# Kernel optimization log

Hardware: AMD Instinct MI355X
Metric: run time of the kernel (lower is better)

## Reference

```python
import jax, jax.numpy as jnp
import numpy as np

N, E = 50000, 800000          # nodes, edges
IN, H, C = 256, 4, 64          # in_channels, heads, per-head out channels
HID, OUT = 64, 40              # lin1 hidden, num classes
NEG_SLOPE = 0.2                # PyG GATConv default


def setup_inputs() -> dict:
    key = jax.random.key(0)
    ks = jax.random.split(key, 10)
    s = 0.05
    return {
        "x": jax.random.normal(ks[0], (N, IN), jnp.float32),
        "edge_index": jax.random.randint(ks[1], (2, E), 0, N, dtype=jnp.int64),
        "W": jax.random.normal(ks[2], (IN, H * C), jnp.float32) * s,     # GATConv lin (no bias)
        "att_src": jax.random.normal(ks[3], (H, C), jnp.float32) * s,
        "att_dst": jax.random.normal(ks[4], (H, C), jnp.float32) * s,
        "bias_conv": jnp.zeros((H * C,), jnp.float32),
        "W1": jax.random.normal(ks[5], (H * C, HID), jnp.float32) * s,
        "b1": jnp.zeros((HID,), jnp.float32),
        "W2": jax.random.normal(ks[6], (HID, OUT), jnp.float32) * s,
        "b2": jnp.zeros((OUT,), jnp.float32),
    }


def reference(x, edge_index, W, att_src, att_dst, bias_conv, W1, b1, W2, b2):
    n = x.shape[0]
    # PyG GATConv default: add self-loops (also guarantees no empty segments)
    loop = jnp.arange(n, dtype=edge_index.dtype)
    src = jnp.concatenate([edge_index[0], loop])  # [E+N]
    dst = jnp.concatenate([edge_index[1], loop])

    h = (x @ W).reshape(n, H, C)                         # [N,H,C]
    a_src = jnp.einsum('nhc,hc->nh', h, att_src)         # [N,H]
    a_dst = jnp.einsum('nhc,hc->nh', h, att_dst)

    # per-edge attention logits + segment softmax over incoming edges of dst
    e = jax.nn.leaky_relu(a_src[src] + a_dst[dst], NEG_SLOPE)   # [E+N,H]
    m = jax.ops.segment_max(e, dst, num_segments=n)             # [N,H]
    ex = jnp.exp(e - m[dst])
    denom = jax.ops.segment_sum(ex, dst, num_segments=n)
    alpha = ex / denom[dst]                                     # [E+N,H]

    # weighted scatter-aggregate of source features
    msg = alpha[:, :, None] * h[src]                            # [E+N,H,C]
    out = jax.ops.segment_sum(msg, dst, num_segments=n)         # [N,H,C]
    out = out.reshape(n, H * C) + bias_conv

    out = jax.nn.relu(out)              # .relu() after conv1 (dropout off in eval)
    out = jax.nn.relu(out @ W1 + b1)    # lin1 + relu
    return out @ W2 + b2                # lin2
```

## Files before the change

### kernel.cpp

```cpp
#include <hip/hip_runtime.h>
#include <math.h>

#define HEADS 4
#define CH 64
#define HC 256
#define SLOPE 0.2f
#define SLOT 64

typedef __attribute__((ext_vector_type(8))) short bf16x8;
typedef __attribute__((ext_vector_type(8))) unsigned short u16x8;
typedef __attribute__((ext_vector_type(4))) float f32x4;

__device__ __forceinline__ float4 ld4(const float* p){ return *(const float4*)p; }
__device__ __forceinline__ void st4(float* p, float4 v){ *(float4*)p = v; }
__device__ __forceinline__ float lrelu(float x){ return x > 0.f ? x : SLOPE * x; }
__device__ __forceinline__ unsigned short f2bf(float f){
  union { float f; unsigned int u; } v; v.f = f;
  unsigned int r = v.u + 0x7fffu + ((v.u >> 16) & 1u);
  return (unsigned short)(r >> 16);
}
__device__ __forceinline__ float bflo(unsigned int u){
  union { unsigned int u; float f; } v; v.u = u << 16; return v.f;
}
__device__ __forceinline__ float bfhi(unsigned int u){
  union { unsigned int u; float f; } v; v.u = u & 0xffff0000u; return v.f;
}
__device__ __forceinline__ void split2(float v, unsigned short& h, unsigned short& l){
  unsigned int u = __float_as_uint(v);
  h = (unsigned short)(u >> 16);
  float hf = __uint_as_float(u & 0xffff0000u);
  l = (unsigned short)(__float_as_uint(v - hf) >> 16);
}
__device__ __forceinline__ void dma16(const unsigned short* g, unsigned short* l){
  __builtin_amdgcn_global_load_lds(
      (const __attribute__((address_space(1))) unsigned int*)g,
      (__attribute__((address_space(3))) unsigned int*)l, 16, 0, 0);
}

__global__ __launch_bounds__(256) void k_pre(
    const float* __restrict__ W, const float* __restrict__ W1, const float* __restrict__ W2,
    unsigned short* __restrict__ Bhi, unsigned short* __restrict__ Blo,
    unsigned short* __restrict__ W1h, unsigned short* __restrict__ W1l,
    unsigned short* __restrict__ W2h, unsigned short* __restrict__ W2l,
    int* __restrict__ cnt, int Nn) {
  int b = blockIdx.x, t = threadIdx.x;
  if (b < 256) {
    int nn = b;
    unsigned short h, l;
    split2(W[(size_t)t*256 + nn], h, l);
    Bhi[(size_t)nn*256 + t] = h; Blo[(size_t)nn*256 + t] = l;
  } else if (b < 320) {
    int nn = b - 256;
    unsigned short h, l;
    split2(W1[(size_t)t*64 + nn], h, l);
    W1h[(size_t)nn*256 + t] = h; W1l[(size_t)nn*256 + t] = l;
  } else if (b < 368) {
    if (t < 64) {
      int nn = b - 320;
      float v = (nn < 40) ? W2[(size_t)t*40 + nn] : 0.f;
      unsigned short h, l;
      split2(v, h, l);
      W2h[(size_t)nn*64 + t] = h; W2l[(size_t)nn*64 + t] = l;
    }
  } else {
    int i = (b - 368)*256 + t;
    if (i < Nn) cnt[i] = 0;
  }
}

__global__ __launch_bounds__(256, 4) void k_gemmfill(const float* __restrict__ x,
    const unsigned short* __restrict__ Bhi_t, const unsigned short* __restrict__ Blo_t,
    unsigned short* __restrict__ hbf,
    const float* __restrict__ att_src, const float* __restrict__ att_dst,
    float* __restrict__ a_srcO, float* __restrict__ a_dstO, int M, int nFill,
    const int* __restrict__ ei, int* __restrict__ cnt, unsigned short* __restrict__ csrf,
    int E, int EN) {
  __shared__ __align__(16) unsigned short L[4*4096];
  int t = threadIdx.x;
  int b = blockIdx.x;
  if (b < nFill) {
    int base = b*2048 + t;
    int s0=0,d0=0,s1=0,d1=0,s2=0,d2=0,s3=0,d3=0;
    int s4=0,d4=0,s5=0,d5=0,s6=0,d6=0,s7=0,d7=0;
    int e0=base, e1=base+256, e2=base+512, e3=base+768;
    int e4=base+1024, e5=base+1280, e6=base+1536, e7=base+1792;
    bool q0=e0<EN,q1=e1<EN,q2=e2<EN,q3=e3<EN,q4=e4<EN,q5=e5<EN,q6=e6<EN,q7=e7<EN;
    if (q0) { if (e0<E) { s0=ei[e0]; d0=ei[E+e0]; } else { s0=e0-E; d0=s0; } }
    if (q1) { if (e1<E) { s1=ei[e1]; d1=ei[E+e1]; } else { s1=e1-E; d1=s1; } }
    if (q2) { if (e2<E) { s2=ei[e2]; d2=ei[E+e2]; } else { s2=e2-E; d2=s2; } }
    if (q3) { if (e3<E) { s3=ei[e3]; d3=ei[E+e3]; } else { s3=e3-E; d3=s3; } }
    if (q4) { if (e4<E) { s4=ei[e4]; d4=ei[E+e4]; } else { s4=e4-E; d4=s4; } }
    if (q5) { if (e5<E) { s5=ei[e5]; d5=ei[E+e5]; } else { s5=e5-E; d5=s5; } }
    if (q6) { if (e6<E) { s6=ei[e6]; d6=ei[E+e6]; } else { s6=e6-E; d6=s6; } }
    if (q7) { if (e7<E) { s7=ei[e7]; d7=ei[E+e7]; } else { s7=e7-E; d7=s7; } }
    if (q0) { int p = atomicAdd(&cnt[d0], 1); csrf[(d0<<6) + p] = (unsigned short)s0; }
    if (q1) { int p = atomicAdd(&cnt[d1], 1); csrf[(d1<<6) + p] = (unsigned short)s1; }
    if (q2) { int p = atomicAdd(&cnt[d2], 1); csrf[(d2<<6) + p] = (unsigned short)s2; }
    if (q3) { int p = atomicAdd(&cnt[d3], 1); csrf[(d3<<6) + p] = (unsigned short)s3; }
    if (q4) { int p = atomicAdd(&cnt[d4], 1); csrf[(d4<<6) + p] = (unsigned short)s4; }
    if (q5) { int p = atomicAdd(&cnt[d5], 1); csrf[(d5<<6) + p] = (unsigned short)s5; }
    if (q6) { int p = atomicAdd(&cnt[d6], 1); csrf[(d6<<6) + p] = (unsigned short)s6; }
    if (q7) { int p = atomicAdd(&cnt[d7], 1); csrf[(d7<<6) + p] = (unsigned short)s7; }
    return;
  }
  int gb = b - nFill;
  int lane = t & 63, w = t >> 6;
  int wr = w >> 1, wc = w & 1;
  int ln15 = lane & 15, lq = lane >> 4;
  int row0 = (gb >> 1) * 128, col0 = (gb & 1) * 128;

  f32x4 acc[4][4];
  #pragma unroll
  for (int i=0;i<4;i++)
    #pragma unroll
    for (int j=0;j<4;j++) acc[i][j] = (f32x4){0.f,0.f,0.f,0.f};

  int sA = w*128 + lane;
  int sB = sA + 64;
  int RA = sA>>3, uA = (sA&7)^(RA&7), idxA = (RA<<1)|(uA&1), segA = uA>>1;
  int RB = sB>>3, uB = (sB&7)^(RB&7), idxB = (RB<<1)|(uB&1), segB = uB>>1;
  size_t gB_a = (size_t)(col0+idxA)*256 + segA*8;
  size_t gB_b = (size_t)(col0+idxB)*256 + segB*8;
  int l0 = (w*128)*8, l1 = (w*128+64)*8;

  int ar = t >> 1, akh = t & 1;
  int arow = row0 + ar;
  bool avalid = arow < M;
  const float* xp = &x[(size_t)arow*256 + akh*16];
  int aR = ar >> 1;
  int u0w = ((2*akh+0) << 1) | (ar & 1);
  int u1w = ((2*akh+1) << 1) | (ar & 1);
  int as0 = aR*8 + (u0w ^ (aR & 7));
  int as1 = aR*8 + (u1w ^ (aR & 7));

  for (int c = 0; c < 8; c++) {
    int k0 = c*32;
    dma16(Bhi_t + gB_a + k0, &L[2*4096 + l0]);
    dma16(Bhi_t + gB_b + k0, &L[2*4096 + l1]);
    dma16(Blo_t + gB_a + k0, &L[3*4096 + l0]);
    dma16(Blo_t + gB_b + k0, &L[3*4096 + l1]);
    float4 f0 = make_float4(0,0,0,0), f1 = f0, f2 = f0, f3 = f0;
    if (avalid) {
      const float* xc = xp + k0;
      f0 = ld4(xc); f1 = ld4(xc+4); f2 = ld4(xc+8); f3 = ld4(xc+12);
    }
    u16x8 h0, l0v, h1, l1v;
    unsigned short hh, ll;
    split2(f0.x,hh,ll); h0[0]=hh; l0v[0]=ll;
    split2(f0.y,hh,ll); h0[1]=hh; l0v[1]=ll;
    split2(f0.z,hh,ll); h0[2]=hh; l0v[2]=ll;
    split2(f0.w,hh,ll); h0[3]=hh; l0v[3]=ll;
    split2(f1.x,hh,ll); h0[4]=hh; l0v[4]=ll;
    split2(f1.y,hh,ll); h0[5]=hh; l0v[5]=ll;
    split2(f1.z,hh,ll); h0[6]=hh; l0v[6]=ll;
    split2(f1.w,hh,ll); h0[7]=hh; l0v[7]=ll;
    split2(f2.x,hh,ll); h1[0]=hh; l1v[0]=ll;
    split2(f2.y,hh,ll); h1[1]=hh; l1v[1]=ll;
    split2(f2.z,hh,ll); h1[2]=hh; l1v[2]=ll;
    split2(f2.w,hh,ll); h1[3]=hh; l1v[3]=ll;
    split2(f3.x,hh,ll); h1[4]=hh; l1v[4]=ll;
    split2(f3.y,hh,ll); h1[5]=hh; l1v[5]=ll;
    split2(f3.z,hh,ll); h1[6]=hh; l1v[6]=ll;
    split2(f3.w,hh,ll); h1[7]=hh; l1v[7]=ll;
    *(u16x8*)&L[0*4096 + as0*8] = h0;
    *(u16x8*)&L[1*4096 + as0*8] = l0v;
    *(u16x8*)&L[0*4096 + as1*8] = h1;
    *(u16x8*)&L[1*4096 + as1*8] = l1v;
    __syncthreads();

    bf16x8 bh[4], bl[4];
    #pragma unroll
    for (int j = 0; j < 4; j++) {
      int nn = wc*64 + j*16 + ln15;
      int R = nn >> 1, u = (lq << 1) | (nn & 1);
      int s = R*8 + (u ^ (R & 7));
      bh[j] = *(bf16x8*)&L[2*4096 + s*8];
      bl[j] = *(bf16x8*)&L[3*4096 + s*8];
    }
    #pragma unroll
    for (int i = 0; i < 4; i++) {
      int r = wr*64 + i*16 + ln15;
      int R = r >> 1, u = (lq << 1) | (r & 1);
      int s = R*8 + (u ^ (R & 7));
      bf16x8 ah = *(bf16x8*)&L[0*4096 + s*8];
      bf16x8 al = *(bf16x8*)&L[1*4096 + s*8];
      #pragma unroll
      for (int j = 0; j < 4; j++) {
        acc[i][j] = __builtin_amdgcn_mfma_f32_16x16x32_bf16(ah, bh[j], acc[i][j], 0,0,0);
        acc[i][j] = __builtin_amdgcn_mfma_f32_16x16x32_bf16(al, bh[j], acc[i][j], 0,0,0);
        acc[i][j] = __builtin_amdgcn_mfma_f32_16x16x32_bf16(ah, bl[j], acc[i][j], 0,0,0);
      }
    }
    __syncthreads();
  }
  unsigned short* hb2 = hbf + (size_t)(gb & 1) * M * 128;
  #pragma unroll
  for (int i = 0; i < 4; i++) {
    #pragma unroll
    for (int r = 0; r < 4; r++) {
      int row = row0 + wr*64 + i*16 + lq*4 + r;
      if (row < M) {
        #pragma unroll
        for (int j = 0; j < 4; j++) {
          int col = wc*64 + j*16 + ln15;
          hb2[(size_t)row*128 + col] = f2bf(acc[i][j][r]);
        }
      }
    }
  }
  int head = (gb & 1)*2 + wc;
  float asv[4], adv[4];
  #pragma unroll
  for (int j=0;j<4;j++){
    asv[j] = att_src[head*CH + j*16 + ln15];
    adv[j] = att_dst[head*CH + j*16 + ln15];
  }
  #pragma unroll
  for (int i = 0; i < 4; i++) {
    #pragma unroll
    for (int r = 0; r < 4; r++) {
      float ps = acc[i][0][r]*asv[0] + acc[i][1][r]*asv[1]
               + acc[i][2][r]*asv[2] + acc[i][3][r]*asv[3];
      float pd = acc[i][0][r]*adv[0] + acc[i][1][r]*adv[1]
               + acc[i][2][r]*adv[2] + acc[i][3][r]*adv[3];
      #pragma unroll
      for (int m=8; m>=1; m>>=1) { ps += __shfl_xor(ps, m); pd += __shfl_xor(pd, m); }
      if (ln15 == 0) {
        int row = row0 + wr*64 + i*16 + lq*4 + r;
        if (row < M) { a_srcO[row*4+head] = ps; a_dstO[row*4+head] = pd; }
      }
    }
  }
}

__global__ __launch_bounds__(256) void k_gat(const unsigned short* __restrict__ hbf,
    const float* __restrict__ a_src, const float* __restrict__ a_dst,
    const int* __restrict__ cnt, const unsigned short* __restrict__ csrf,
    const float* __restrict__ bias, unsigned short* __restrict__ outbf,
    int N, int nBlk) {
  int w = threadIdx.x >> 6, lane = threadIdx.x & 63;
  int q = lane >> 4, cl = lane & 15;
  int pass = (blockIdx.x >= nBlk) ? 1 : 0;
  int blk = blockIdx.x - pass*nBlk;
  int n = blk*16 + w*4 + q;
  int c0 = cl * 8;
  int hd = cl >> 3;
  int eb = q * 16;
  const unsigned short* hb = hbf + (size_t)pass * N * 128;
  const unsigned short* row = &csrf[(size_t)n << 6];

  __shared__ float s_p[4][64][2];

  float2 ad = *(const float2*)&a_dst[(size_t)n*4 + pass*2];
  float dsum = 0.f;
  float acc[8];
  #pragma unroll
  for (int k=0;k<8;k++) acc[k]=0.f;

  int deg = cnt[n];
  int dm = max(deg, __shfl_xor(deg, 16));
  dm = max(dm, __shfl_xor(dm, 32));

  for (int cb = 0; cb < dm; cb += 16) {
    int cnt16 = min(16, deg - cb);
    int cm  = min(16, dm - cb);
    int s = 0;
    float p0 = 0.f, p1 = 0.f;
    if (cl < cnt16) {
      s = row[cb + cl];
      float2 as = *(const float2*)&a_src[(size_t)s*4 + pass*2];
      p0 = __expf(lrelu(as.x + ad.x));
      p1 = __expf(lrelu(as.y + ad.y));
    }
    *(float2*)&s_p[w][eb + cl][0] = make_float2(p0, p1);

    bool v0 = 0 < cnt16, v1 = 1 < cnt16, v2 = 2 < cnt16, v3 = 3 < cnt16;
    uint4 u0 = make_uint4(0,0,0,0), u1 = u0, u2 = u0, u3 = u0;
    int ss;
    ss = __shfl(s, eb + 0); if (v0) u0 = *(const uint4*)&hb[(size_t)ss*128 + c0];
    ss = __shfl(s, eb + 1); if (v1) u1 = *(const uint4*)&hb[(size_t)ss*128 + c0];
    ss = __shfl(s, eb + 2); if (v2) u2 = *(const uint4*)&hb[(size_t)ss*128 + c0];
    ss = __shfl(s, eb + 3); if (v3) u3 = *(const uint4*)&hb[(size_t)ss*128 + c0];
    for (int g = 0; g < cm; g += 4) {
      int f0 = g+4, f1 = g+5, f2 = g+6, f3 = g+7;
      bool w0 = f0 < cnt16, w1 = f1 < cnt16, w2 = f2 < cnt16, w3 = f3 < cnt16;
      uint4 t0 = make_uint4(0,0,0,0), t1 = t0, t2 = t0, t3 = t0;
      ss = __shfl(s, eb + (f0 & 15)); if (w0) t0 = *(const uint4*)&hb[(size_t)ss*128 + c0];
      ss = __shfl(s, eb + (f1 & 15)); if (w1) t1 = *(const uint4*)&hb[(size_t)ss*128 + c0];
      ss = __shfl(s, eb + (f2 & 15)); if (w2) t2 = *(const uint4*)&hb[(size_t)ss*128 + c0];
      ss = __shfl(s, eb + (f3 & 15)); if (w3) t3 = *(const uint4*)&hb[(size_t)ss*128 + c0];
      if (v0) {
        float pw = s_p[w][eb + g    ][hd]; dsum += pw;
        acc[0] += pw*bflo(u0.x); acc[1] += pw*bfhi(u0.x);
        acc[2] += pw*bflo(u0.y); acc[3] += pw*bfhi(u0.y);
        acc[4] += pw*bflo(u0.z); acc[5] += pw*bfhi(u0.z);
        acc[6] += pw*bflo(u0.w); acc[7] += pw*bfhi(u0.w);
      }
      if (v1) {
        float pw = s_p[w][eb + g + 1][hd]; dsum += pw;
        acc[0] += pw*bflo(u1.x); acc[1] += pw*bfhi(u1.x);
        acc[2] += pw*bflo(u1.y); acc[3] += pw*bfhi(u1.y);
        acc[4] += pw*bflo(u1.z); acc[5] += pw*bfhi(u1.z);
        acc[6] += pw*bflo(u1.w); acc[7] += pw*bfhi(u1.w);
      }
      if (v2) {
        float pw = s_p[w][eb + g + 2][hd]; dsum += pw;
        acc[0] += pw*bflo(u2.x); acc[1] += pw*bfhi(u2.x);
        acc[2] += pw*bflo(u2.y); acc[3] += pw*bfhi(u2.y);
        acc[4] += pw*bflo(u2.z); acc[5] += pw*bfhi(u2.z);
        acc[6] += pw*bflo(u2.w); acc[7] += pw*bfhi(u2.w);
      }
      if (v3) {
        float pw = s_p[w][eb + g + 3][hd]; dsum += pw;
        acc[0] += pw*bflo(u3.x); acc[1] += pw*bfhi(u3.x);
        acc[2] += pw*bflo(u3.y); acc[3] += pw*bfhi(u3.y);
        acc[4] += pw*bflo(u3.z); acc[5] += pw*bfhi(u3.z);
        acc[6] += pw*bflo(u3.w); acc[7] += pw*bfhi(u3.w);
      }
      u0 = t0; u1 = t1; u2 = t2; u3 = t3;
      v0 = w0; v1 = w1; v2 = w2; v3 = w3;
    }
  }
  float inv = 1.f / dsum;
  float4 b0 = ld4(&bias[pass*128 + c0]);
  float4 b1 = ld4(&bias[pass*128 + c0 + 4]);
  uint4 o;
  o.x = (unsigned)f2bf(fmaxf(acc[0]*inv + b0.x, 0.f))
      | ((unsigned)f2bf(fmaxf(acc[1]*inv + b0.y, 0.f)) << 16);
  o.y = (unsigned)f2bf(fmaxf(acc[2]*inv + b0.z, 0.f))
      | ((unsigned)f2bf(fmaxf(acc[3]*inv + b0.w, 0.f)) << 16);
  o.z = (unsigned)f2bf(fmaxf(acc[4]*inv + b1.x, 0.f))
      | ((unsigned)f2bf(fmaxf(acc[5]*inv + b1.y, 0.f)) << 16);
  o.w = (unsigned)f2bf(fmaxf(acc[6]*inv + b1.z, 0.f))
      | ((unsigned)f2bf(fmaxf(acc[7]*inv + b1.w, 0.f)) << 16);
  *(uint4*)&outbf[(size_t)n*HC + pass*128 + c0] = o;
}

__global__ __launch_bounds__(256) void k_mlp(const unsigned short* __restrict__ Cbf,
    const unsigned short* __restrict__ W1h, const unsigned short* __restrict__ W1l,
    const unsigned short* __restrict__ W2h, const unsigned short* __restrict__ W2l,
    const float* __restrict__ b1, const float* __restrict__ b2,
    float* __restrict__ out, int M) {
  __shared__ __align__(16) unsigned short Hs[64*72];
  int t = threadIdx.x, lane = t & 63, w = t >> 6;
  int ln15 = lane & 15, lq = lane >> 4;
  int row0 = blockIdx.x * 64;
  int arow = row0 + w*16 + ln15;

  bf16x8 a[8];
  bool av = arow < M;
  const unsigned short* ap = &Cbf[(size_t)arow*256 + lq*8];
  #pragma unroll
  for (int kf = 0; kf < 8; kf++) {
    if (av) a[kf] = *(const bf16x8*)(ap + kf*32);
    else    a[kf] = (bf16x8){0,0,0,0,0,0,0,0};
  }

  f32x4 acc1[4];
  #pragma unroll
  for (int j=0;j<4;j++) acc1[j] = (f32x4){0.f,0.f,0.f,0.f};

  #pragma unroll
  for (int kf = 0; kf < 8; kf++) {
    int k = kf*32 + lq*8;
    #pragma unroll
    for (int j = 0; j < 4; j++) {
      int n = j*16 + ln15;
      bf16x8 bh = *(const bf16x8*)&W1h[(size_t)n*256 + k];
      bf16x8 bl = *(const bf16x8*)&W1l[(size_t)n*256 + k];
      acc1[j] = __builtin_amdgcn_mfma_f32_16x16x32_bf16(a[kf], bh, acc1[j], 0,0,0);
      acc1[j] = __builtin_amdgcn_mfma_f32_16x16x32_bf16(a[kf], bl, acc1[j], 0,0,0);
    }
  }
  #pragma unroll
  for (int j = 0; j < 4; j++) {
    int col = j*16 + ln15;
    float bv = b1[col];
    #pragma unroll
    for (int r = 0; r < 4; r++) {
      int rl = w*16 + lq*4 + r;
      Hs[rl*72 + col] = f2bf(fmaxf(acc1[j][r] + bv, 0.f));
    }
  }
  __syncthreads();
  f32x4 acc2[3];
  #pragma unroll
  for (int j=0;j<3;j++) acc2[j] = (f32x4){0.f,0.f,0.f,0.f};
  #pragma unroll
  for (int kf = 0; kf < 2; kf++) {
    int m = w*16 + ln15;
    bf16x8 a2 = *(bf16x8*)&Hs[m*72 + kf*32 + lq*8];
    #pragma unroll
    for (int j = 0; j < 3; j++) {
      int n = j*16 + ln15;
      int k = kf*32 + lq*8;
      bf16x8 wh = *(const bf16x8*)&W2h[(size_t)n*64 + k];
      bf16x8 wl = *(const bf16x8*)&W2l[(size_t)n*64 + k];
      acc2[j] = __builtin_amdgcn_mfma_f32_16x16x32_bf16(a2, wh, acc2[j], 0,0,0);
      acc2[j] = __builtin_amdgcn_mfma_f32_16x16x32_bf16(a2, wl, acc2[j], 0,0,0);
    }
  }
  #pragma unroll
  for (int j = 0; j < 3; j++) {
    int col = j*16 + ln15;
    if (col < 40) {
      float bv = b2[col];
      #pragma unroll
      for (int r = 0; r < 4; r++) {
        int row = row0 + w*16 + lq*4 + r;
        if (row < M) out[(size_t)row*40 + col] = acc2[j][r] + bv;
      }
    }
  }
}

extern "C" void kernel_launch(void* const* d_in, const int* in_sizes, int n_in,
                              void* d_out, int out_size, void* d_ws, size_t ws_size,
                              hipStream_t stream) {
  const int Nn = in_sizes[0] / HC;
  const int E  = in_sizes[1] / 2;
  const int Mpad = (Nn + 127) & ~127;
  const float* x        = (const float*)d_in[0];
  const int*   ei       = (const int*)d_in[1];
  const float* W        = (const float*)d_in[2];
  const float* att_src  = (const float*)d_in[3];
  const float* att_dst  = (const float*)d_in[4];
  const float* biasconv = (const float*)d_in[5];
  const float* W1       = (const float*)d_in[6];
  const float* b1       = (const float*)d_in[7];
  const float* W2       = (const float*)d_in[8];
  const float* b2       = (const float*)d_in[9];
  float* out = (float*)d_out;

  size_t off = 0;
  auto alloc = [&](size_t bytes)->void* {
    void* p = (void*)((char*)d_ws + off);
    off += (bytes + 255) & ~(size_t)255;
    return p;
  };
  unsigned short* hbf  = (unsigned short*)alloc((size_t)Nn*HC*sizeof(unsigned short));
  unsigned short* outc = (unsigned short*)alloc((size_t)Mpad*HC*sizeof(unsigned short));
  unsigned short* Bhi = (unsigned short*)alloc((size_t)256*256*sizeof(unsigned short));
  unsigned short* Blo = (unsigned short*)alloc((size_t)256*256*sizeof(unsigned short));
  unsigned short* W1h = (unsigned short*)alloc((size_t)64*256*sizeof(unsigned short));
  unsigned short* W1l = (unsigned short*)alloc((size_t)64*256*sizeof(unsigned short));
  unsigned short* W2h = (unsigned short*)alloc((size_t)48*64*sizeof(unsigned short));
  unsigned short* W2l = (unsigned short*)alloc((size_t)48*64*sizeof(unsigned short));
  float* a_src_v  = (float*)alloc((size_t)Nn*4*sizeof(float));
  float* a_dst_v  = (float*)alloc((size_t)Nn*4*sizeof(float));
  int*   cnt      = (int*)alloc((size_t)Nn*sizeof(int));
  unsigned short* csrf = (unsigned short*)alloc((size_t)Nn*SLOT*sizeof(unsigned short));
  (void)ws_size; (void)n_in; (void)out_size;

  dim3 blk(256);
  int nGemm = 2 * (Mpad/128);
  int EN = E + Nn;
  int nFill = (EN + 2047)/2048;
  int nZero = (Nn + 255)/256;
  int nBlkGat = Nn/16;

  k_pre<<<dim3(368 + nZero), blk, 0, stream>>>(W, W1, W2,
      Bhi, Blo, W1h, W1l, W2h, W2l, cnt, Nn);
  k_gemmfill<<<dim3(nFill + nGemm), blk, 0, stream>>>(x, Bhi, Blo, hbf,
      att_src, att_dst, a_src_v, a_dst_v, Nn, nFill, ei, cnt, csrf, E, EN);
  k_gat<<<dim3(2*nBlkGat), blk, 0, stream>>>(hbf, a_src_v, a_dst_v,
                                             cnt, csrf, biasconv, outc, Nn, nBlkGat);
  k_mlp<<<dim3((Mpad + 63)/64), blk, 0, stream>>>(outc, W1h, W1l, W2h, W2l, b1, b2, out, Nn);
}
```

Measured before the change: 267.7 us.

## Widen CSR slots to int32 and stage MLP input via LDS DMA

The bucketed CSR neighbor array changes from 16-bit to 32-bit indices, which roughly doubles that buffer's footprint and traffic but stores source ids without truncation. The MLP kernel no longer loads each row's whole A-fragment into registers up front. It now streams 32-column chunks into a swizzled shared buffer with async DMA, synchronising around each chunk, which trades register pressure for extra barriers. The MLP grid now uses Mpad/64 blocks with no row-bounds check on loads.

```diff
diff --git a/kernel.cpp b/kernel.cpp
--- a/kernel.cpp
+++ b/kernel.cpp
@@ -73,7 +73,7 @@
     unsigned short* __restrict__ hbf,
     const float* __restrict__ att_src, const float* __restrict__ att_dst,
     float* __restrict__ a_srcO, float* __restrict__ a_dstO, int M, int nFill,
-    const int* __restrict__ ei, int* __restrict__ cnt, unsigned short* __restrict__ csrf,
+    const int* __restrict__ ei, int* __restrict__ cnt, int* __restrict__ csrf,
     int E, int EN) {
   __shared__ __align__(16) unsigned short L[4*4096];
   int t = threadIdx.x;
@@ -93,14 +93,14 @@
     if (q5) { if (e5<E) { s5=ei[e5]; d5=ei[E+e5]; } else { s5=e5-E; d5=s5; } }
     if (q6) { if (e6<E) { s6=ei[e6]; d6=ei[E+e6]; } else { s6=e6-E; d6=s6; } }
     if (q7) { if (e7<E) { s7=ei[e7]; d7=ei[E+e7]; } else { s7=e7-E; d7=s7; } }
-    if (q0) { int p = atomicAdd(&cnt[d0], 1); csrf[(d0<<6) + p] = (unsigned short)s0; }
-    if (q1) { int p = atomicAdd(&cnt[d1], 1); csrf[(d1<<6) + p] = (unsigned short)s1; }
-    if (q2) { int p = atomicAdd(&cnt[d2], 1); csrf[(d2<<6) + p] = (unsigned short)s2; }
-    if (q3) { int p = atomicAdd(&cnt[d3], 1); csrf[(d3<<6) + p] = (unsigned short)s3; }
-    if (q4) { int p = atomicAdd(&cnt[d4], 1); csrf[(d4<<6) + p] = (unsigned short)s4; }
-    if (q5) { int p = atomicAdd(&cnt[d5], 1); csrf[(d5<<6) + p] = (unsigned short)s5; }
-    if (q6) { int p = atomicAdd(&cnt[d6], 1); csrf[(d6<<6) + p] = (unsigned short)s6; }
-    if (q7) { int p = atomicAdd(&cnt[d7], 1); csrf[(d7<<6) + p] = (unsigned short)s7; }
+    if (q0) { int p = atomicAdd(&cnt[d0], 1); csrf[(d0<<6) + p] = s0; }
+    if (q1) { int p = atomicAdd(&cnt[d1], 1); csrf[(d1<<6) + p] = s1; }
+    if (q2) { int p = atomicAdd(&cnt[d2], 1); csrf[(d2<<6) + p] = s2; }
+    if (q3) { int p = atomicAdd(&cnt[d3], 1); csrf[(d3<<6) + p] = s3; }
+    if (q4) { int p = atomicAdd(&cnt[d4], 1); csrf[(d4<<6) + p] = s4; }
+    if (q5) { int p = atomicAdd(&cnt[d5], 1); csrf[(d5<<6) + p] = s5; }
+    if (q6) { int p = atomicAdd(&cnt[d6], 1); csrf[(d6<<6) + p] = s6; }
+    if (q7) { int p = atomicAdd(&cnt[d7], 1); csrf[(d7<<6) + p] = s7; }
     return;
   }
   int gb = b - nFill;
@@ -235,7 +235,7 @@
 
 __global__ __launch_bounds__(256) void k_gat(const unsigned short* __restrict__ hbf,
     const float* __restrict__ a_src, const float* __restrict__ a_dst,
-    const int* __restrict__ cnt, const unsigned short* __restrict__ csrf,
+    const int* __restrict__ cnt, const int* __restrict__ csrf,
     const float* __restrict__ bias, unsigned short* __restrict__ outbf,
     int N, int nBlk) {
   int w = threadIdx.x >> 6, lane = threadIdx.x & 63;
@@ -247,7 +247,7 @@
   int hd = cl >> 3;
   int eb = q * 16;
   const unsigned short* hb = hbf + (size_t)pass * N * 128;
-  const unsigned short* row = &csrf[(size_t)n << 6];
+  const int* row = &csrf[(size_t)n << 6];
 
   __shared__ float s_p[4][64][2];
 
@@ -341,36 +341,37 @@
     const unsigned short* __restrict__ W2h, const unsigned short* __restrict__ W2l,
     const float* __restrict__ b1, const float* __restrict__ b2,
     float* __restrict__ out, int M) {
+  __shared__ __align__(16) unsigned short Abuf[2048];
   __shared__ __align__(16) unsigned short Hs[64*72];
   int t = threadIdx.x, lane = t & 63, w = t >> 6;
   int ln15 = lane & 15, lq = lane >> 4;
   int row0 = blockIdx.x * 64;
-  int arow = row0 + w*16 + ln15;
-
-  bf16x8 a[8];
-  bool av = arow < M;
-  const unsigned short* ap = &Cbf[(size_t)arow*256 + lq*8];
-  #pragma unroll
-  for (int kf = 0; kf < 8; kf++) {
-    if (av) a[kf] = *(const bf16x8*)(ap + kf*32);
-    else    a[kf] = (bf16x8){0,0,0,0,0,0,0,0};
-  }
 
   f32x4 acc1[4];
   #pragma unroll
   for (int j=0;j<4;j++) acc1[j] = (f32x4){0.f,0.f,0.f,0.f};
 
-  #pragma unroll
-  for (int kf = 0; kf < 8; kf++) {
-    int k = kf*32 + lq*8;
+  int sA = t;
+  int rA = sA >> 2, segA = (sA & 3) ^ ((rA >> 1) & 3);
+  size_t gA = (size_t)(row0 + rA) * 256 + segA*8;
+
+  for (int c = 0; c < 8; c++) {
+    int k0 = c*32;
+    dma16(Cbf + gA + k0, &Abuf[sA*8]);
+    __syncthreads();
+    int r = w*16 + ln15;
+    int s = r*4 + (lq ^ ((r >> 1) & 3));
+    bf16x8 a = *(bf16x8*)&Abuf[s*8];
     #pragma unroll
     for (int j = 0; j < 4; j++) {
       int n = j*16 + ln15;
+      int k = k0 + lq*8;
       bf16x8 bh = *(const bf16x8*)&W1h[(size_t)n*256 + k];
       bf16x8 bl = *(const bf16x8*)&W1l[(size_t)n*256 + k];
-      acc1[j] = __builtin_amdgcn_mfma_f32_16x16x32_bf16(a[kf], bh, acc1[j], 0,0,0);
-      acc1[j] = __builtin_amdgcn_mfma_f32_16x16x32_bf16(a[kf], bl, acc1[j], 0,0,0);
-    }
+      acc1[j] = __builtin_amdgcn_mfma_f32_16x16x32_bf16(a, bh, acc1[j], 0,0,0);
+      acc1[j] = __builtin_amdgcn_mfma_f32_16x16x32_bf16(a, bl, acc1[j], 0,0,0);
+    }
+    __syncthreads();
   }
   #pragma unroll
   for (int j = 0; j < 4; j++) {
@@ -382,7 +383,6 @@
       Hs[rl*72 + col] = f2bf(fmaxf(acc1[j][r] + bv, 0.f));
     }
   }
-  __syncthreads();
   f32x4 acc2[3];
   #pragma unroll
   for (int j=0;j<3;j++) acc2[j] = (f32x4){0.f,0.f,0.f,0.f};
@@ -449,7 +449,7 @@
   float* a_src_v  = (float*)alloc((size_t)Nn*4*sizeof(float));
   float* a_dst_v  = (float*)alloc((size_t)Nn*4*sizeof(float));
   int*   cnt      = (int*)alloc((size_t)Nn*sizeof(int));
-  unsigned short* csrf = (unsigned short*)alloc((size_t)Nn*SLOT*sizeof(unsigned short));
+  int*   csrf     = (int*)alloc((size_t)Nn*SLOT*sizeof(int));
   (void)ws_size; (void)n_in; (void)out_size;
 
   dim3 blk(256);
@@ -465,5 +465,5 @@
       att_src, att_dst, a_src_v, a_dst_v, Nn, nFill, ei, cnt, csrf, E, EN);
   k_gat<<<dim3(2*nBlkGat), blk, 0, stream>>>(hbf, a_src_v, a_dst_v,
                                              cnt, csrf, biasconv, outc, Nn, nBlkGat);
-  k_mlp<<<dim3((Mpad + 63)/64), blk, 0, stream>>>(outc, W1h, W1l, W2h, W2l, b1, b2, out, Nn);
-}
+  k_mlp<<<dim3(Mpad/64), blk, 0, stream>>>(outc, W1h, W1l, W2h, W2l, b1, b2, out, Nn);
+}
```

Result: no change. 268.0 us (+0.1%).
